# Optimization experiments

Measured on AMD Instinct MI355X. Metric: run time of the kernel, lower is better.

## Reference

```python
import jax, jax.numpy as jnp
import numpy as np

RADIUS = 1.0


def setup_inputs() -> dict:
    key = jax.random.key(0)
    ks = jax.random.split(key, 9)
    Nq, No, P, L = 1024, 2048, 3, 64
    pos_query = jax.random.uniform(ks[0], (Nq, P), dtype=jnp.float32)
    pos_obs = jax.random.uniform(ks[1], (No, P), dtype=jnp.float32)
    h_obs = jax.random.normal(ks[2], (No, L), dtype=jnp.float32)
    # kernel_mlp: Linear(3*P, L) -> ReLU -> Linear(L, 1)
    W1 = jax.random.normal(ks[3], (3 * P, L), dtype=jnp.float32) * (1.0 / np.sqrt(3 * P))
    b1 = jnp.zeros((L,), jnp.float32)
    W2 = jax.random.normal(ks[4], (L, 1), dtype=jnp.float32) * (1.0 / np.sqrt(L))
    b2 = jnp.zeros((1,), jnp.float32)
    # value_proj: Linear(L, L)
    Wv = jax.random.normal(ks[5], (L, L), dtype=jnp.float32) * (1.0 / np.sqrt(L))
    bv = jnp.zeros((L,), jnp.float32)
    obs_mask = jnp.ones((No,), jnp.int32)
    obs_batch = jnp.sort(jax.random.randint(ks[6], (No,), 0, 4, dtype=jnp.int32))
    query_batch = jnp.sort(jax.random.randint(ks[7], (Nq,), 0, 4, dtype=jnp.int32))
    return dict(h_obs=h_obs, pos_obs=pos_obs, pos_query=pos_query,
                W1=W1, b1=b1, W2=W2, b2=b2, Wv=Wv, bv=bv,
                obs_mask=obs_mask, obs_batch=obs_batch, query_batch=query_batch)


def reference(h_obs, pos_obs, pos_query, W1, b1, W2, b2, Wv, bv,
              obs_mask, obs_batch, query_batch):
    Nq, P = pos_query.shape
    No = pos_obs.shape[0]
    rel = pos_query[:, None, :] - pos_obs[None, :, :]                 # [Nq,No,P]
    kin = jnp.concatenate([
        jnp.broadcast_to(pos_query[:, None, :], (Nq, No, P)),
        jnp.broadcast_to(pos_obs[None, :, :], (Nq, No, P)),
        rel,
    ], axis=-1)                                                        # [Nq,No,3P]
    hidden = jax.nn.relu(jnp.einsum('qop,pl->qol', kin, W1) + b1)      # [Nq,No,L]
    logits = jnp.einsum('qol,lk->qok', hidden, W2)[..., 0] + b2[0]     # [Nq,No]
    # masks: same batch, within radius, observed
    same = query_batch[:, None] == obs_batch[None, :]
    dist = jnp.linalg.norm(rel, axis=-1)
    mask = same & (dist <= RADIUS) & (obs_mask[None, :] != 0)
    # masked softmax over obs dim; fully-masked rows -> all-zero weights
    # (matches torch softmax(-inf row) -> nan -> nan_to_num(0))
    logits_safe = jnp.where(mask, logits, 0.0)
    m = jnp.max(jnp.where(mask, logits, -jnp.inf), axis=1, keepdims=True)
    m = jnp.where(jnp.isfinite(m), m, 0.0)
    e = jnp.where(mask, jnp.exp(logits_safe - m), 0.0)
    denom = jnp.sum(e, axis=1, keepdims=True)
    weights = e / jnp.maximum(denom, 1e-30)                            # [Nq,No]
    v = h_obs @ Wv + bv                                                # [No,L]
    return weights @ v                                                 # [Nq,L]
```

## Files before the change

### kernel.cpp

```cpp
#include <hip/hip_runtime.h>
#include <math.h>

#define LDIM 64
#define QT2 32
#define QW 8
#define LOG2E 1.4426950408889634f

static __device__ __forceinline__ float fast_exp2(float x) {
#if __has_builtin(__builtin_amdgcn_exp2f)
    return __builtin_amdgcn_exp2f(x);
#else
    return exp2f(x);
#endif
}

static __device__ __forceinline__ float4 ld4(const float* p) {
    return *(const float4*)p;
}

__global__ __launch_bounds__(256) void gano_accum(
    const float* __restrict__ h_obs,
    const float* __restrict__ pos_obs, const float* __restrict__ pos_query,
    const float* __restrict__ W1, const float* __restrict__ b1,
    const float* __restrict__ W2,
    const int* __restrict__ obs_mask, const int* __restrict__ obs_batch,
    const int* __restrict__ query_batch,
    float* __restrict__ acc, float* __restrict__ den,
    int No, int Nq)
{
    const int c   = blockIdx.x;
    const int q0  = blockIdx.y * QT2;
    const int tid = threadIdx.x, lane = tid & 63, wid = tid >> 6;

    if ((c << 6) >= No) return;
    const int c_lo = obs_batch[c << 6];
    const int c_hi = obs_batch[min((c << 6) + 63, No - 1)];
    if (c_lo > query_batch[min(q0 + QT2 - 1, Nq - 1)] || c_hi < query_batch[q0]) return;

    __shared__ float4 B4[16][64];
    __shared__ float4 a4[QT2][16];
    __shared__ float4 w2_4[16];
    __shared__ float4 qp4[QT2];
    __shared__ float  e_lds[QT2][LDIM];

    if (tid < QT2) {
        const int q = min(q0 + tid, Nq - 1);
        qp4[tid] = make_float4(pos_query[q*3+0], pos_query[q*3+1], pos_query[q*3+2],
                               (float)(query_batch[q] + 1));
    }
    if (tid < 16) {
        const float4 w = ld4(W2 + 4 * tid);
        w2_4[tid] = make_float4(w.x * LOG2E, w.y * LOG2E, w.z * LOG2E, w.w * LOG2E);
    }
    for (int i = tid; i < QT2 * 16; i += 256) {
        const int q = i >> 4, g = i & 15;
        const int qq = min(q0 + q, Nq - 1);
        const float px = pos_query[qq*3+0], py = pos_query[qq*3+1], pz = pos_query[qq*3+2];
        const float4 u0 = ld4(W1 + 0*LDIM + 4*g), u6 = ld4(W1 + 6*LDIM + 4*g);
        const float4 u1 = ld4(W1 + 1*LDIM + 4*g), u7 = ld4(W1 + 7*LDIM + 4*g);
        const float4 u2 = ld4(W1 + 2*LDIM + 4*g), u8 = ld4(W1 + 8*LDIM + 4*g);
        float4 r;
        r.x = fmaf(px, u0.x+u6.x, fmaf(py, u1.x+u7.x, pz*(u2.x+u8.x)));
        r.y = fmaf(px, u0.y+u6.y, fmaf(py, u1.y+u7.y, pz*(u2.y+u8.y)));
        r.z = fmaf(px, u0.z+u6.z, fmaf(py, u1.z+u7.z, pz*(u2.z+u8.z)));
        r.w = fmaf(px, u0.w+u6.w, fmaf(py, u1.w+u7.w, pz*(u2.w+u8.w)));
        a4[q][g] = r;
    }
    const int oo = (c << 6) + lane;
    float px = 0.f, py = 0.f, pz = 0.f, pcode = 0.f;
    if (oo < No) {
        px = pos_obs[oo*3+0]; py = pos_obs[oo*3+1]; pz = pos_obs[oo*3+2];
        pcode = obs_mask[oo] ? (float)(obs_batch[oo] + 1) : 0.0f;
    }
    #pragma unroll
    for (int k = 0; k < 4; ++k) {
        const int g = (wid + k * 4) & 15;
        const float4 b0 = ld4(b1 + 4*g);
        const float4 u3 = ld4(W1 + 3*LDIM + 4*g), u6 = ld4(W1 + 6*LDIM + 4*g);
        const float4 u4 = ld4(W1 + 4*LDIM + 4*g), u7 = ld4(W1 + 7*LDIM + 4*g);
        const float4 u5 = ld4(W1 + 5*LDIM + 4*g), u8 = ld4(W1 + 8*LDIM + 4*g);
        float4 r;
        r.x = fmaf(px, u3.x-u6.x, fmaf(py, u4.x-u7.x, fmaf(pz, u5.x-u8.x, b0.x)));
        r.y = fmaf(px, u3.y-u6.y, fmaf(py, u4.y-u7.y, fmaf(pz, u5.y-u8.y, b0.y)));
        r.z = fmaf(px, u3.z-u6.z, fmaf(py, u4.z-u7.z, fmaf(pz, u5.z-u8.z, b0.z)));
        r.w = fmaf(px, u3.w-u6.w, fmaf(py, u4.w-u7.w, fmaf(pz, u5.w-u8.w, b0.w)));
        B4[g][lane] = r;
    }
    __syncthreads();

    float lgq[QW];
    #pragma unroll
    for (int j = 0; j < QW; ++j) lgq[j] = 0.0f;
    #pragma unroll
    for (int g = 0; g < 16; ++g) {
        const float4 Bv = B4[g][lane];
        const float4 w  = w2_4[g];
        #pragma unroll
        for (int j = 0; j < QW; ++j) {
            const float4 a = a4[wid * QW + j][g];
            lgq[j] = fmaf(fmaxf(a.x + Bv.x, 0.f), w.x, lgq[j]);
            lgq[j] = fmaf(fmaxf(a.y + Bv.y, 0.f), w.y, lgq[j]);
            lgq[j] = fmaf(fmaxf(a.z + Bv.z, 0.f), w.z, lgq[j]);
            lgq[j] = fmaf(fmaxf(a.w + Bv.w, 0.f), w.w, lgq[j]);
        }
    }

    float ds[QW];
    #pragma unroll
    for (int j = 0; j < QW; ++j) {
        const float4 qp = qp4[wid * QW + j];
        const float dx = qp.x - px, dy = qp.y - py, dz = qp.z - pz;
        const float d2 = fmaf(dz, dz, fmaf(dy, dy, dx * dx));
        const bool valid = (pcode == qp.w) & (d2 <= 1.0f);
        const float e = valid ? fast_exp2(lgq[j]) : 0.0f;
        e_lds[wid * QW + j][lane] = e;
        ds[j] = e;
    }
    #pragma unroll
    for (int msk = 32; msk; msk >>= 1) {
        #pragma unroll
        for (int j = 0; j < QW; ++j) ds[j] += __shfl_xor(ds[j], msk, 64);
    }
    if (lane == 0) {
        #pragma unroll
        for (int j = 0; j < QW; ++j) atomicAdd(&den[q0 + wid * QW + j], ds[j]);
    }

    float pacc[QW];
    #pragma unroll
    for (int j = 0; j < QW; ++j) pacc[j] = 0.0f;
    const float* Hc = h_obs + ((size_t)c << 12) + lane;
    if ((c << 6) + 64 <= No) {
        for (int o2 = 0; o2 < LDIM; o2 += 4) {
            const float v0 = Hc[(o2 + 0) << 6];
            const float v1 = Hc[(o2 + 1) << 6];
            const float v2 = Hc[(o2 + 2) << 6];
            const float v3 = Hc[(o2 + 3) << 6];
            #pragma unroll
            for (int j = 0; j < QW; ++j) {
                const float4 e = *(const float4*)&e_lds[wid * QW + j][o2];
                pacc[j] = fmaf(e.x, v0, pacc[j]);
                pacc[j] = fmaf(e.y, v1, pacc[j]);
                pacc[j] = fmaf(e.z, v2, pacc[j]);
                pacc[j] = fmaf(e.w, v3, pacc[j]);
            }
        }
    } else {
        for (int o2 = 0; o2 < LDIM; ++o2) {
            const int orow = min((c << 6) + o2, No - 1);
            const float v0 = h_obs[((size_t)orow << 6) + lane];
            #pragma unroll
            for (int j = 0; j < QW; ++j)
                pacc[j] = fmaf(e_lds[wid * QW + j][o2], v0, pacc[j]);
        }
    }
    #pragma unroll
    for (int j = 0; j < QW; ++j)
        atomicAdd(&acc[(size_t)(q0 + wid * QW + j) * LDIM + lane], pacc[j]);
}

__global__ __launch_bounds__(256) void gano_norm(
    const float* __restrict__ acc, const float* __restrict__ den,
    const float* __restrict__ Wv, const float* __restrict__ bv,
    float* __restrict__ out, int Nq)
{
    const int tid = threadIdx.x, lane = tid & 63, wid = tid >> 6;
    const int q0 = blockIdx.x * 8 + wid * 2;
    if (q0 >= Nq) return;

    __shared__ float r_lds[4][2][LDIM];

    const float D0 = den[q0];
    const float D1 = (q0 + 1 < Nq) ? den[q0 + 1] : 0.0f;
    const float rd0 = (D0 > 0.0f) ? 1.0f / D0 : 0.0f;
    const float rd1 = (D1 > 0.0f) ? 1.0f / D1 : 0.0f;
    r_lds[wid][0][lane] = acc[(size_t)q0 * LDIM + lane] * rd0;
    r_lds[wid][1][lane] = (q0 + 1 < Nq) ? acc[(size_t)(q0 + 1) * LDIM + lane] * rd1 : 0.0f;
    float o0 = 0.f, o1 = 0.f;
    #pragma unroll 8
    for (int k = 0; k < LDIM; ++k) {
        const float w = Wv[(k << 6) + lane];
        o0 = fmaf(r_lds[wid][0][k], w, o0);
        o1 = fmaf(r_lds[wid][1][k], w, o1);
    }
    const float b = bv[lane];
    out[(size_t)q0 * LDIM + lane] = (D0 > 0.0f) ? o0 + b : 0.0f;
    if (q0 + 1 < Nq)
        out[(size_t)(q0 + 1) * LDIM + lane] = (D1 > 0.0f) ? o1 + b : 0.0f;
}

extern "C" void kernel_launch(void* const* d_in, const int* in_sizes, int n_in,
                              void* d_out, int out_size, void* d_ws, size_t ws_size,
                              hipStream_t stream) {
    const float* h_obs     = (const float*)d_in[0];
    const float* pos_obs   = (const float*)d_in[1];
    const float* pos_query = (const float*)d_in[2];
    const float* W1        = (const float*)d_in[3];
    const float* b1        = (const float*)d_in[4];
    const float* W2        = (const float*)d_in[5];
    const float* Wv        = (const float*)d_in[7];
    const float* bv        = (const float*)d_in[8];
    const int* obs_mask    = (const int*)d_in[9];
    const int* obs_batch   = (const int*)d_in[10];
    const int* query_batch = (const int*)d_in[11];

    const int No     = in_sizes[1] / 3;
    const int Nq     = in_sizes[2] / 3;
    const int NoA    = (No + 63) & ~63;
    const int nC     = NoA / 64;
    const int nTiles = (Nq + QT2 - 1) / QT2;

    float* acc = (float*)d_ws;
    float* den = acc + (size_t)Nq * LDIM;

    hipMemsetAsync(acc, 0, (size_t)Nq * (LDIM + 1) * sizeof(float), stream);

    dim3 g1(nC, nTiles);
    gano_accum<<<g1, 256, 0, stream>>>(
        h_obs, pos_obs, pos_query, W1, b1, W2,
        obs_mask, obs_batch, query_batch,
        acc, den, No, Nq);

    gano_norm<<<(Nq + 7) / 8, 256, 0, stream>>>(acc, den, Wv, bv, (float*)d_out, Nq);
}
```

Measured before the change: 31.92 us.

## Precompute MLP partials in prepass and loop obs chunks per query tile

Adds a prepass kernel that computes the per-observation and per-query first-layer partials, packed positions, and scaled W2 once. The same prepass finds, by binary search, the observation-chunk window for each 8-query tile and zeroes the accumulators, which replaces the memset. The accumulate kernel now uses 64-thread blocks over (12 strided slots × query tiles) and loops over only the chunks in that tile's batch window, accumulating locally before one set of atomics. The aim is to cut redundant recomputation, empty blocks and atomic traffic. In exchange it adds global round trips for the precomputed buffers and gives less parallelism per block.

```diff
diff --git a/kernel.cpp b/kernel.cpp
--- a/kernel.cpp
+++ b/kernel.cpp
@@ -2,8 +2,8 @@
 #include <math.h>
 
 #define LDIM 64
-#define QT2 32
-#define QW 8
+#define QTW 8
+#define WMAX 12
 #define LOG2E 1.4426950408889634f
 
 static __device__ __forceinline__ float fast_exp2(float x) {
@@ -18,44 +18,38 @@
     return *(const float4*)p;
 }
 
-__global__ __launch_bounds__(256) void gano_accum(
-    const float* __restrict__ h_obs,
+__global__ __launch_bounds__(256) void gano_pre(
     const float* __restrict__ pos_obs, const float* __restrict__ pos_query,
     const float* __restrict__ W1, const float* __restrict__ b1,
     const float* __restrict__ W2,
     const int* __restrict__ obs_mask, const int* __restrict__ obs_batch,
     const int* __restrict__ query_batch,
-    float* __restrict__ acc, float* __restrict__ den,
-    int No, int Nq)
+    float4* __restrict__ Bi, float4* __restrict__ A4, float4* __restrict__ P4,
+    float4* __restrict__ w2s4, int2* __restrict__ qwin, float* __restrict__ zeroR,
+    int No, int NoA, int Nq, int nC, int nQT, int zn)
 {
-    const int c   = blockIdx.x;
-    const int q0  = blockIdx.y * QT2;
-    const int tid = threadIdx.x, lane = tid & 63, wid = tid >> 6;
-
-    if ((c << 6) >= No) return;
-    const int c_lo = obs_batch[c << 6];
-    const int c_hi = obs_batch[min((c << 6) + 63, No - 1)];
-    if (c_lo > query_batch[min(q0 + QT2 - 1, Nq - 1)] || c_hi < query_batch[q0]) return;
-
-    __shared__ float4 B4[16][64];
-    __shared__ float4 a4[QT2][16];
-    __shared__ float4 w2_4[16];
-    __shared__ float4 qp4[QT2];
-    __shared__ float  e_lds[QT2][LDIM];
-
-    if (tid < QT2) {
-        const int q = min(q0 + tid, Nq - 1);
-        qp4[tid] = make_float4(pos_query[q*3+0], pos_query[q*3+1], pos_query[q*3+2],
-                               (float)(query_batch[q] + 1));
-    }
-    if (tid < 16) {
-        const float4 w = ld4(W2 + 4 * tid);
-        w2_4[tid] = make_float4(w.x * LOG2E, w.y * LOG2E, w.z * LOG2E, w.w * LOG2E);
-    }
-    for (int i = tid; i < QT2 * 16; i += 256) {
-        const int q = i >> 4, g = i & 15;
-        const int qq = min(q0 + q, Nq - 1);
-        const float px = pos_query[qq*3+0], py = pos_query[qq*3+1], pz = pos_query[qq*3+2];
+    const int gid = blockIdx.x * blockDim.x + threadIdx.x;
+
+    if (gid < NoA * 16) {
+        const int o = gid & 63, g = (gid >> 6) & 15, c = gid >> 10;
+        const int oo = (c << 6) + o;
+        float4 r = make_float4(0.f, 0.f, 0.f, 0.f);
+        if (oo < No) {
+            const float px = pos_obs[oo*3+0], py = pos_obs[oo*3+1], pz = pos_obs[oo*3+2];
+            const float4 b0 = ld4(b1 + 4*g);
+            const float4 u3 = ld4(W1 + 3*LDIM + 4*g), u6 = ld4(W1 + 6*LDIM + 4*g);
+            const float4 u4 = ld4(W1 + 4*LDIM + 4*g), u7 = ld4(W1 + 7*LDIM + 4*g);
+            const float4 u5 = ld4(W1 + 5*LDIM + 4*g), u8 = ld4(W1 + 8*LDIM + 4*g);
+            r.x = fmaf(px, u3.x-u6.x, fmaf(py, u4.x-u7.x, fmaf(pz, u5.x-u8.x, b0.x)));
+            r.y = fmaf(px, u3.y-u6.y, fmaf(py, u4.y-u7.y, fmaf(pz, u5.y-u8.y, b0.y)));
+            r.z = fmaf(px, u3.z-u6.z, fmaf(py, u4.z-u7.z, fmaf(pz, u5.z-u8.z, b0.z)));
+            r.w = fmaf(px, u3.w-u6.w, fmaf(py, u4.w-u7.w, fmaf(pz, u5.w-u8.w, b0.w)));
+        }
+        Bi[gid] = r;
+    }
+    if (gid < Nq * 16) {
+        const int q = gid >> 4, g = gid & 15;
+        const float px = pos_query[q*3+0], py = pos_query[q*3+1], pz = pos_query[q*3+2];
         const float4 u0 = ld4(W1 + 0*LDIM + 4*g), u6 = ld4(W1 + 6*LDIM + 4*g);
         const float4 u1 = ld4(W1 + 1*LDIM + 4*g), u7 = ld4(W1 + 7*LDIM + 4*g);
         const float4 u2 = ld4(W1 + 2*LDIM + 4*g), u8 = ld4(W1 + 8*LDIM + 4*g);
@@ -64,99 +58,154 @@
         r.y = fmaf(px, u0.y+u6.y, fmaf(py, u1.y+u7.y, pz*(u2.y+u8.y)));
         r.z = fmaf(px, u0.z+u6.z, fmaf(py, u1.z+u7.z, pz*(u2.z+u8.z)));
         r.w = fmaf(px, u0.w+u6.w, fmaf(py, u1.w+u7.w, pz*(u2.w+u8.w)));
-        a4[q][g] = r;
-    }
-    const int oo = (c << 6) + lane;
-    float px = 0.f, py = 0.f, pz = 0.f, pcode = 0.f;
-    if (oo < No) {
-        px = pos_obs[oo*3+0]; py = pos_obs[oo*3+1]; pz = pos_obs[oo*3+2];
-        pcode = obs_mask[oo] ? (float)(obs_batch[oo] + 1) : 0.0f;
-    }
+        A4[gid] = r;
+    }
+    if (gid < NoA) {
+        float4 pp = make_float4(0.f, 0.f, 0.f, 0.f);
+        if (gid < No)
+            pp = make_float4(pos_obs[gid*3+0], pos_obs[gid*3+1], pos_obs[gid*3+2],
+                             obs_mask[gid] ? (float)(obs_batch[gid] + 1) : 0.0f);
+        P4[gid] = pp;
+    }
+    if (gid < 16) {
+        const float4 w = ld4(W2 + 4 * gid);
+        w2s4[gid] = make_float4(w.x * LOG2E, w.y * LOG2E, w.z * LOG2E, w.w * LOG2E);
+    }
+    if (gid < nQT) {
+        const int q0 = gid * QTW;
+        const int t_lo = query_batch[min(q0, Nq - 1)];
+        const int t_hi = query_batch[min(q0 + QTW - 1, Nq - 1)];
+        int lo = 0, hi = nC;
+        while (lo < hi) { int mid = (lo + hi) >> 1;
+            if (obs_batch[min(mid * 64 + 63, No - 1)] < t_lo) lo = mid + 1; else hi = mid; }
+        const int cs = lo;
+        lo = 0; hi = nC;
+        while (lo < hi) { int mid = (lo + hi) >> 1;
+            if (obs_batch[min(mid * 64, No - 1)] <= t_hi) lo = mid + 1; else hi = mid; }
+        qwin[gid] = make_int2(cs, lo - 1);
+    }
+    if (gid < zn) zeroR[gid] = 0.0f;
+}
+
+__global__ __launch_bounds__(64) void gano_accum(
+    const float* __restrict__ h_obs,
+    const float4* __restrict__ Bi, const float4* __restrict__ A4,
+    const float4* __restrict__ P4, const float4* __restrict__ w2s4,
+    const float* __restrict__ pos_query, const int* __restrict__ query_batch,
+    const int2* __restrict__ qwin,
+    float* __restrict__ acc, float* __restrict__ den,
+    int No, int Nq)
+{
+    const int rel = blockIdx.x;
+    const int qt  = blockIdx.y;
+    const int q0  = qt * QTW;
+    const int lane = threadIdx.x;
+
+    const int2 w = qwin[qt];
+    if (w.x + rel > w.y) return;
+
+    __shared__ float4 a4[QTW][16];
+    __shared__ float4 w2l[16];
+    __shared__ float4 qp4[QTW];
+    __shared__ float  e_lds[QTW][LDIM];
+
+    if (lane < 16) w2l[lane] = w2s4[lane];
+    if (lane < QTW) {
+        const int q = min(q0 + lane, Nq - 1);
+        qp4[lane] = make_float4(pos_query[q*3+0], pos_query[q*3+1], pos_query[q*3+2],
+                                (float)(query_batch[q] + 1));
+    }
+    {
+        const int i0 = lane, i1 = lane + 64;
+        a4[i0 >> 4][i0 & 15] = A4[(size_t)q0 * 16 + i0];
+        a4[i1 >> 4][i1 & 15] = A4[(size_t)q0 * 16 + i1];
+    }
+
+    float den_a[QTW], pacc[QTW];
     #pragma unroll
-    for (int k = 0; k < 4; ++k) {
-        const int g = (wid + k * 4) & 15;
-        const float4 b0 = ld4(b1 + 4*g);
-        const float4 u3 = ld4(W1 + 3*LDIM + 4*g), u6 = ld4(W1 + 6*LDIM + 4*g);
-        const float4 u4 = ld4(W1 + 4*LDIM + 4*g), u7 = ld4(W1 + 7*LDIM + 4*g);
-        const float4 u5 = ld4(W1 + 5*LDIM + 4*g), u8 = ld4(W1 + 8*LDIM + 4*g);
-        float4 r;
-        r.x = fmaf(px, u3.x-u6.x, fmaf(py, u4.x-u7.x, fmaf(pz, u5.x-u8.x, b0.x)));
-        r.y = fmaf(px, u3.y-u6.y, fmaf(py, u4.y-u7.y, fmaf(pz, u5.y-u8.y, b0.y)));
-        r.z = fmaf(px, u3.z-u6.z, fmaf(py, u4.z-u7.z, fmaf(pz, u5.z-u8.z, b0.z)));
-        r.w = fmaf(px, u3.w-u6.w, fmaf(py, u4.w-u7.w, fmaf(pz, u5.w-u8.w, b0.w)));
-        B4[g][lane] = r;
-    }
-    __syncthreads();
-
-    float lgq[QW];
+    for (int j = 0; j < QTW; ++j) { den_a[j] = 0.0f; pacc[j] = 0.0f; }
+
+    for (int c = w.x + rel; c <= w.y; c += WMAX) {
+        const float4 p = P4[(c << 6) + lane];
+        const float4* Bc = Bi + ((size_t)c << 10) + lane;
+
+        float lg[QTW];
+        #pragma unroll
+        for (int j = 0; j < QTW; ++j) lg[j] = 0.0f;
+        #pragma unroll
+        for (int g = 0; g < 16; ++g) {
+            const float4 Bv = Bc[g << 6];
+            const float4 wv = w2l[g];
+            #pragma unroll
+            for (int j = 0; j < QTW; ++j) {
+                const float4 a = a4[j][g];
+                lg[j] = fmaf(fmaxf(a.x + Bv.x, 0.f), wv.x, lg[j]);
+                lg[j] = fmaf(fmaxf(a.y + Bv.y, 0.f), wv.y, lg[j]);
+                lg[j] = fmaf(fmaxf(a.z + Bv.z, 0.f), wv.z, lg[j]);
+                lg[j] = fmaf(fmaxf(a.w + Bv.w, 0.f), wv.w, lg[j]);
+            }
+        }
+
+        #pragma unroll
+        for (int j = 0; j < QTW; ++j) {
+            const float4 qp = qp4[j];
+            const float dx = qp.x - p.x, dy = qp.y - p.y, dz = qp.z - p.z;
+            const float d2 = fmaf(dz, dz, fmaf(dy, dy, dx * dx));
+            const bool valid = (p.w == qp.w) & (d2 <= 1.0f);
+            const float e = valid ? fast_exp2(lg[j]) : 0.0f;
+            e_lds[j][lane] = e;
+            lg[j] = e;
+        }
+        #pragma unroll
+        for (int msk = 32; msk; msk >>= 1) {
+            #pragma unroll
+            for (int j = 0; j < QTW; ++j) lg[j] += __shfl_xor(lg[j], msk, 64);
+        }
+        #pragma unroll
+        for (int j = 0; j < QTW; ++j) den_a[j] += lg[j];
+
+        const float* Hc = h_obs + ((size_t)c << 12) + lane;
+        if ((c << 6) + 64 <= No) {
+            for (int oo = 0; oo < LDIM; oo += 8) {
+                const float v0 = Hc[(oo + 0) << 6];
+                const float v1 = Hc[(oo + 1) << 6];
+                const float v2 = Hc[(oo + 2) << 6];
+                const float v3 = Hc[(oo + 3) << 6];
+                const float v4 = Hc[(oo + 4) << 6];
+                const float v5 = Hc[(oo + 5) << 6];
+                const float v6 = Hc[(oo + 6) << 6];
+                const float v7 = Hc[(oo + 7) << 6];
+                #pragma unroll
+                for (int j = 0; j < QTW; ++j) {
+                    const float4 ea = *(const float4*)&e_lds[j][oo];
+                    const float4 eb = *(const float4*)&e_lds[j][oo + 4];
+                    float s = pacc[j];
+                    s = fmaf(ea.x, v0, s); s = fmaf(ea.y, v1, s);
+                    s = fmaf(ea.z, v2, s); s = fmaf(ea.w, v3, s);
+                    s = fmaf(eb.x, v4, s); s = fmaf(eb.y, v5, s);
+                    s = fmaf(eb.z, v6, s); s = fmaf(eb.w, v7, s);
+                    pacc[j] = s;
+                }
+            }
+        } else {
+            for (int oo = 0; oo < LDIM; ++oo) {
+                const int orow = min((c << 6) + oo, No - 1);
+                const float v = h_obs[((size_t)orow << 6) + lane];
+                #pragma unroll
+                for (int j = 0; j < QTW; ++j)
+                    pacc[j] = fmaf(e_lds[j][oo], v, pacc[j]);
+            }
+        }
+    }
+
+    if (lane == 0) {
+        #pragma unroll
+        for (int j = 0; j < QTW; ++j)
+            if (q0 + j < Nq) atomicAdd(&den[q0 + j], den_a[j]);
+    }
     #pragma unroll
-    for (int j = 0; j < QW; ++j) lgq[j] = 0.0f;
-    #pragma unroll
-    for (int g = 0; g < 16; ++g) {
-        const float4 Bv = B4[g][lane];
-        const float4 w  = w2_4[g];
-        #pragma unroll
-        for (int j = 0; j < QW; ++j) {
-            const float4 a = a4[wid * QW + j][g];
-            lgq[j] = fmaf(fmaxf(a.x + Bv.x, 0.f), w.x, lgq[j]);
-            lgq[j] = fmaf(fmaxf(a.y + Bv.y, 0.f), w.y, lgq[j]);
-            lgq[j] = fmaf(fmaxf(a.z + Bv.z, 0.f), w.z, lgq[j]);
-            lgq[j] = fmaf(fmaxf(a.w + Bv.w, 0.f), w.w, lgq[j]);
-        }
-    }
-
-    float ds[QW];
-    #pragma unroll
-    for (int j = 0; j < QW; ++j) {
-        const float4 qp = qp4[wid * QW + j];
-        const float dx = qp.x - px, dy = qp.y - py, dz = qp.z - pz;
-        const float d2 = fmaf(dz, dz, fmaf(dy, dy, dx * dx));
-        const bool valid = (pcode == qp.w) & (d2 <= 1.0f);
-        const float e = valid ? fast_exp2(lgq[j]) : 0.0f;
-        e_lds[wid * QW + j][lane] = e;
-        ds[j] = e;
-    }
-    #pragma unroll
-    for (int msk = 32; msk; msk >>= 1) {
-        #pragma unroll
-        for (int j = 0; j < QW; ++j) ds[j] += __shfl_xor(ds[j], msk, 64);
-    }
-    if (lane == 0) {
-        #pragma unroll
-        for (int j = 0; j < QW; ++j) atomicAdd(&den[q0 + wid * QW + j], ds[j]);
-    }
-
-    float pacc[QW];
-    #pragma unroll
-    for (int j = 0; j < QW; ++j) pacc[j] = 0.0f;
-    const float* Hc = h_obs + ((size_t)c << 12) + lane;
-    if ((c << 6) + 64 <= No) {
-        for (int o2 = 0; o2 < LDIM; o2 += 4) {
-            const float v0 = Hc[(o2 + 0) << 6];
-            const float v1 = Hc[(o2 + 1) << 6];
-            const float v2 = Hc[(o2 + 2) << 6];
-            const float v3 = Hc[(o2 + 3) << 6];
-            #pragma unroll
-            for (int j = 0; j < QW; ++j) {
-                const float4 e = *(const float4*)&e_lds[wid * QW + j][o2];
-                pacc[j] = fmaf(e.x, v0, pacc[j]);
-                pacc[j] = fmaf(e.y, v1, pacc[j]);
-                pacc[j] = fmaf(e.z, v2, pacc[j]);
-                pacc[j] = fmaf(e.w, v3, pacc[j]);
-            }
-        }
-    } else {
-        for (int o2 = 0; o2 < LDIM; ++o2) {
-            const int orow = min((c << 6) + o2, No - 1);
-            const float v0 = h_obs[((size_t)orow << 6) + lane];
-            #pragma unroll
-            for (int j = 0; j < QW; ++j)
-                pacc[j] = fmaf(e_lds[wid * QW + j][o2], v0, pacc[j]);
-        }
-    }
-    #pragma unroll
-    for (int j = 0; j < QW; ++j)
-        atomicAdd(&acc[(size_t)(q0 + wid * QW + j) * LDIM + lane], pacc[j]);
+    for (int j = 0; j < QTW; ++j)
+        if (q0 + j < Nq) atomicAdd(&acc[(size_t)(q0 + j) * LDIM + lane], pacc[j]);
 }
 
 __global__ __launch_bounds__(256) void gano_norm(
@@ -204,21 +253,32 @@
     const int* obs_batch   = (const int*)d_in[10];
     const int* query_batch = (const int*)d_in[11];
 
-    const int No     = in_sizes[1] / 3;
-    const int Nq     = in_sizes[2] / 3;
-    const int NoA    = (No + 63) & ~63;
-    const int nC     = NoA / 64;
-    const int nTiles = (Nq + QT2 - 1) / QT2;
-
-    float* acc = (float*)d_ws;
-    float* den = acc + (size_t)Nq * LDIM;
-
-    hipMemsetAsync(acc, 0, (size_t)Nq * (LDIM + 1) * sizeof(float), stream);
-
-    dim3 g1(nC, nTiles);
-    gano_accum<<<g1, 256, 0, stream>>>(
-        h_obs, pos_obs, pos_query, W1, b1, W2,
-        obs_mask, obs_batch, query_batch,
+    const int No  = in_sizes[1] / 3;
+    const int Nq  = in_sizes[2] / 3;
+    const int NoA = (No + 63) & ~63;
+    const int nC  = NoA / 64;
+    const int nQT = (Nq + QTW - 1) / QTW;
+    const int zn  = Nq * (LDIM + 1);
+
+    float4* Bi   = (float4*)d_ws;
+    float4* A4   = Bi + (size_t)NoA * 16;
+    float4* P4   = A4 + (size_t)Nq * 16;
+    float4* w2s4 = P4 + NoA;
+    int2*   qwin = (int2*)(w2s4 + 16);
+    float*  acc  = (float*)(qwin + nQT);
+    float*  den  = acc + (size_t)Nq * LDIM;
+
+    int gridN = NoA * 16;
+    if (Nq * 16 > gridN) gridN = Nq * 16;
+    if (zn > gridN) gridN = zn;
+
+    gano_pre<<<(gridN + 255) / 256, 256, 0, stream>>>(
+        pos_obs, pos_query, W1, b1, W2, obs_mask, obs_batch, query_batch,
+        Bi, A4, P4, w2s4, qwin, acc, No, NoA, Nq, nC, nQT, zn);
+
+    dim3 g2(WMAX, nQT);
+    gano_accum<<<g2, 64, 0, stream>>>(
+        h_obs, Bi, A4, P4, w2s4, pos_query, query_batch, qwin,
         acc, den, No, Nq);
 
     gano_norm<<<(Nq + 7) / 8, 256, 0, stream>>>(acc, den, Wv, bv, (float*)d_out, Nq);
```

Result: slower. 45.17 us (+41.5%).

## Register-tile h_obs with float4 loads and cut accumulation atomics via shuffle reduce

Applied to the files above, without the earlier changes.

Each lane now owns a 16-obs by 4-channel slice of h_obs, preloaded into registers with float4 loads before the logit computation so the global load latency overlaps the MLP math. The weighted-sum phase uses these register tiles with float4 reads of the exp weights from LDS. Partial sums are then reduced across the four obs groups with shuffles, so only 16 lanes issue atomics per query. The grid is transposed so query tiles vary fastest, and bounds checks on q are added. It costs more registers (64 floats for H4 plus 32 for the accumulators), which may reduce occupancy.

```diff
diff --git a/kernel.cpp b/kernel.cpp
--- a/kernel.cpp
+++ b/kernel.cpp
@@ -2,7 +2,7 @@
 #include <math.h>
 
 #define LDIM 64
-#define QT2 32
+#define QT 32
 #define QW 8
 #define LOG2E 1.4426950408889634f
 
@@ -28,31 +28,27 @@
     float* __restrict__ acc, float* __restrict__ den,
     int No, int Nq)
 {
-    const int c   = blockIdx.x;
-    const int q0  = blockIdx.y * QT2;
+    const int t   = blockIdx.x;
+    const int c   = blockIdx.y;
+    const int q0  = t * QT;
     const int tid = threadIdx.x, lane = tid & 63, wid = tid >> 6;
 
     if ((c << 6) >= No) return;
     const int c_lo = obs_batch[c << 6];
     const int c_hi = obs_batch[min((c << 6) + 63, No - 1)];
-    if (c_lo > query_batch[min(q0 + QT2 - 1, Nq - 1)] || c_hi < query_batch[q0]) return;
+    const int t_lo = query_batch[min(q0, Nq - 1)];
+    const int t_hi = query_batch[min(q0 + QT - 1, Nq - 1)];
+    if (c_lo > t_hi || c_hi < t_lo) return;
 
     __shared__ float4 B4[16][64];
-    __shared__ float4 a4[QT2][16];
-    __shared__ float4 w2_4[16];
-    __shared__ float4 qp4[QT2];
-    __shared__ float  e_lds[QT2][LDIM];
-
-    if (tid < QT2) {
-        const int q = min(q0 + tid, Nq - 1);
-        qp4[tid] = make_float4(pos_query[q*3+0], pos_query[q*3+1], pos_query[q*3+2],
-                               (float)(query_batch[q] + 1));
-    }
-    if (tid < 16) {
-        const float4 w = ld4(W2 + 4 * tid);
-        w2_4[tid] = make_float4(w.x * LOG2E, w.y * LOG2E, w.z * LOG2E, w.w * LOG2E);
-    }
-    for (int i = tid; i < QT2 * 16; i += 256) {
+    __shared__ float4 a4[QT][16];
+    __shared__ float4 w2l[16];
+    __shared__ float4 qp4[QT];
+    __shared__ float  e_lds[4][QW][LDIM];
+
+    #pragma unroll
+    for (int rep = 0; rep < 2; ++rep) {
+        const int i = tid + rep * 256;
         const int q = i >> 4, g = i & 15;
         const int qq = min(q0 + q, Nq - 1);
         const float px = pos_query[qq*3+0], py = pos_query[qq*3+1], pz = pos_query[qq*3+2];
@@ -66,6 +62,15 @@
         r.w = fmaf(px, u0.w+u6.w, fmaf(py, u1.w+u7.w, pz*(u2.w+u8.w)));
         a4[q][g] = r;
     }
+    if (tid < 16) {
+        const float4 w = ld4(W2 + 4 * tid);
+        w2l[tid] = make_float4(w.x * LOG2E, w.y * LOG2E, w.z * LOG2E, w.w * LOG2E);
+    }
+    if (tid < QT) {
+        const int q = min(q0 + tid, Nq - 1);
+        qp4[tid] = make_float4(pos_query[q*3+0], pos_query[q*3+1], pos_query[q*3+2],
+                               (float)(query_batch[q] + 1));
+    }
     const int oo = (c << 6) + lane;
     float px = 0.f, py = 0.f, pz = 0.f, pcode = 0.f;
     if (oo < No) {
@@ -74,7 +79,7 @@
     }
     #pragma unroll
     for (int k = 0; k < 4; ++k) {
-        const int g = (wid + k * 4) & 15;
+        const int g = wid * 4 + k;
         const float4 b0 = ld4(b1 + 4*g);
         const float4 u3 = ld4(W1 + 3*LDIM + 4*g), u6 = ld4(W1 + 6*LDIM + 4*g);
         const float4 u4 = ld4(W1 + 4*LDIM + 4*g), u7 = ld4(W1 + 7*LDIM + 4*g);
@@ -88,75 +93,106 @@
     }
     __syncthreads();
 
-    float lgq[QW];
-    #pragma unroll
-    for (int j = 0; j < QW; ++j) lgq[j] = 0.0f;
+    const int og = lane >> 4, k4 = lane & 15;
+    float4 H4[16];
+    if ((c << 6) + 64 <= No) {
+        const float* Hb = h_obs + (((size_t)(c << 6) + (og << 4)) << 6) + (k4 << 2);
+        #pragma unroll
+        for (int i = 0; i < 16; ++i) H4[i] = ld4(Hb + ((size_t)i << 6));
+    } else {
+        #pragma unroll
+        for (int i = 0; i < 16; ++i) {
+            const int orow = min((c << 6) + (og << 4) + i, No - 1);
+            H4[i] = ld4(h_obs + ((size_t)orow << 6) + (k4 << 2));
+        }
+    }
+
+    float lg[QW];
+    #pragma unroll
+    for (int j = 0; j < QW; ++j) lg[j] = 0.0f;
     #pragma unroll
     for (int g = 0; g < 16; ++g) {
         const float4 Bv = B4[g][lane];
-        const float4 w  = w2_4[g];
+        const float4 wv = w2l[g];
         #pragma unroll
         for (int j = 0; j < QW; ++j) {
             const float4 a = a4[wid * QW + j][g];
-            lgq[j] = fmaf(fmaxf(a.x + Bv.x, 0.f), w.x, lgq[j]);
-            lgq[j] = fmaf(fmaxf(a.y + Bv.y, 0.f), w.y, lgq[j]);
-            lgq[j] = fmaf(fmaxf(a.z + Bv.z, 0.f), w.z, lgq[j]);
-            lgq[j] = fmaf(fmaxf(a.w + Bv.w, 0.f), w.w, lgq[j]);
-        }
-    }
-
-    float ds[QW];
+            lg[j] = fmaf(fmaxf(a.x + Bv.x, 0.f), wv.x, lg[j]);
+            lg[j] = fmaf(fmaxf(a.y + Bv.y, 0.f), wv.y, lg[j]);
+            lg[j] = fmaf(fmaxf(a.z + Bv.z, 0.f), wv.z, lg[j]);
+            lg[j] = fmaf(fmaxf(a.w + Bv.w, 0.f), wv.w, lg[j]);
+        }
+    }
+
+    float den_a[QW];
     #pragma unroll
     for (int j = 0; j < QW; ++j) {
         const float4 qp = qp4[wid * QW + j];
         const float dx = qp.x - px, dy = qp.y - py, dz = qp.z - pz;
         const float d2 = fmaf(dz, dz, fmaf(dy, dy, dx * dx));
         const bool valid = (pcode == qp.w) & (d2 <= 1.0f);
-        const float e = valid ? fast_exp2(lgq[j]) : 0.0f;
-        e_lds[wid * QW + j][lane] = e;
-        ds[j] = e;
-    }
+        const float e = valid ? fast_exp2(lg[j]) : 0.0f;
+        e_lds[wid][j][lane] = e;
+        den_a[j] = e;
+    }
+
+    float4 acc4[QW];
+    #pragma unroll
+    for (int j = 0; j < QW; ++j) acc4[j] = make_float4(0.f, 0.f, 0.f, 0.f);
+    #pragma unroll
+    for (int s = 0; s < 4; ++s) {
+        float4 e4[QW];
+        #pragma unroll
+        for (int j = 0; j < QW; ++j)
+            e4[j] = *(const float4*)&e_lds[wid][j][(og << 4) + (s << 2)];
+        const float4 h0 = H4[(s << 2) + 0];
+        const float4 h1 = H4[(s << 2) + 1];
+        const float4 h2 = H4[(s << 2) + 2];
+        const float4 h3 = H4[(s << 2) + 3];
+        #pragma unroll
+        for (int j = 0; j < QW; ++j) {
+            float4 v = acc4[j];
+            v.x = fmaf(e4[j].x, h0.x, v.x); v.y = fmaf(e4[j].x, h0.y, v.y);
+            v.z = fmaf(e4[j].x, h0.z, v.z); v.w = fmaf(e4[j].x, h0.w, v.w);
+            v.x = fmaf(e4[j].y, h1.x, v.x); v.y = fmaf(e4[j].y, h1.y, v.y);
+            v.z = fmaf(e4[j].y, h1.z, v.z); v.w = fmaf(e4[j].y, h1.w, v.w);
+            v.x = fmaf(e4[j].z, h2.x, v.x); v.y = fmaf(e4[j].z, h2.y, v.y);
+            v.z = fmaf(e4[j].z, h2.z, v.z); v.w = fmaf(e4[j].z, h2.w, v.w);
+            v.x = fmaf(e4[j].w, h3.x, v.x); v.y = fmaf(e4[j].w, h3.y, v.y);
+            v.z = fmaf(e4[j].w, h3.z, v.z); v.w = fmaf(e4[j].w, h3.w, v.w);
+            acc4[j] = v;
+        }
+    }
+
     #pragma unroll
     for (int msk = 32; msk; msk >>= 1) {
         #pragma unroll
-        for (int j = 0; j < QW; ++j) ds[j] += __shfl_xor(ds[j], msk, 64);
+        for (int j = 0; j < QW; ++j) den_a[j] += __shfl_xor(den_a[j], msk, 64);
     }
     if (lane == 0) {
         #pragma unroll
-        for (int j = 0; j < QW; ++j) atomicAdd(&den[q0 + wid * QW + j], ds[j]);
-    }
-
-    float pacc[QW];
-    #pragma unroll
-    for (int j = 0; j < QW; ++j) pacc[j] = 0.0f;
-    const float* Hc = h_obs + ((size_t)c << 12) + lane;
-    if ((c << 6) + 64 <= No) {
-        for (int o2 = 0; o2 < LDIM; o2 += 4) {
-            const float v0 = Hc[(o2 + 0) << 6];
-            const float v1 = Hc[(o2 + 1) << 6];
-            const float v2 = Hc[(o2 + 2) << 6];
-            const float v3 = Hc[(o2 + 3) << 6];
-            #pragma unroll
-            for (int j = 0; j < QW; ++j) {
-                const float4 e = *(const float4*)&e_lds[wid * QW + j][o2];
-                pacc[j] = fmaf(e.x, v0, pacc[j]);
-                pacc[j] = fmaf(e.y, v1, pacc[j]);
-                pacc[j] = fmaf(e.z, v2, pacc[j]);
-                pacc[j] = fmaf(e.w, v3, pacc[j]);
-            }
-        }
-    } else {
-        for (int o2 = 0; o2 < LDIM; ++o2) {
-            const int orow = min((c << 6) + o2, No - 1);
-            const float v0 = h_obs[((size_t)orow << 6) + lane];
-            #pragma unroll
-            for (int j = 0; j < QW; ++j)
-                pacc[j] = fmaf(e_lds[wid * QW + j][o2], v0, pacc[j]);
-        }
-    }
-    #pragma unroll
-    for (int j = 0; j < QW; ++j)
-        atomicAdd(&acc[(size_t)(q0 + wid * QW + j) * LDIM + lane], pacc[j]);
+        for (int j = 0; j < QW; ++j) {
+            const int q = q0 + wid * QW + j;
+            if (q < Nq) atomicAdd(&den[q], den_a[j]);
+        }
+    }
+
+    #pragma unroll
+    for (int j = 0; j < QW; ++j) {
+        float4 v = acc4[j];
+        v.x += __shfl_xor(v.x, 16, 64); v.y += __shfl_xor(v.y, 16, 64);
+        v.z += __shfl_xor(v.z, 16, 64); v.w += __shfl_xor(v.w, 16, 64);
+        v.x += __shfl_xor(v.x, 32, 64); v.y += __shfl_xor(v.y, 32, 64);
+        v.z += __shfl_xor(v.z, 32, 64); v.w += __shfl_xor(v.w, 32, 64);
+        const int q = q0 + wid * QW + j;
+        if (lane < 16 && q < Nq) {
+            float* dst = acc + (size_t)q * LDIM + (k4 << 2);
+            atomicAdd(dst + 0, v.x);
+            atomicAdd(dst + 1, v.y);
+            atomicAdd(dst + 2, v.z);
+            atomicAdd(dst + 3, v.w);
+        }
+    }
 }
 
 __global__ __launch_bounds__(256) void gano_norm(
@@ -204,18 +240,17 @@
     const int* obs_batch   = (const int*)d_in[10];
     const int* query_batch = (const int*)d_in[11];
 
-    const int No     = in_sizes[1] / 3;
-    const int Nq     = in_sizes[2] / 3;
-    const int NoA    = (No + 63) & ~63;
-    const int nC     = NoA / 64;
-    const int nTiles = (Nq + QT2 - 1) / QT2;
+    const int No  = in_sizes[1] / 3;
+    const int Nq  = in_sizes[2] / 3;
+    const int nC  = (No + 63) / 64;
+    const int nT  = (Nq + QT - 1) / QT;
 
     float* acc = (float*)d_ws;
     float* den = acc + (size_t)Nq * LDIM;
 
     hipMemsetAsync(acc, 0, (size_t)Nq * (LDIM + 1) * sizeof(float), stream);
 
-    dim3 g1(nC, nTiles);
+    dim3 g1(nT, nC);
     gano_accum<<<g1, 256, 0, stream>>>(
         h_obs, pos_obs, pos_query, W1, b1, W2,
         obs_mask, obs_batch, query_batch,
```

After: 49.64 us. 55.5% more time.
